# Performance work log

Hardware: AMD Instinct MI355X
Metric: run time of the kernel (lower is better)

## Reference

```python
import jax, jax.numpy as jnp
import numpy as np

D_MODEL = 1024
NUM_HEADS = 16
D_K = D_MODEL // NUM_HEADS


def setup_inputs() -> dict:
    key = jax.random.key(0)
    ks = jax.random.split(key, 5)
    s = 1.0 / np.sqrt(D_MODEL)
    return {
        "x": jax.random.normal(ks[0], (2, 2048, D_MODEL), dtype=jnp.float32),
        "Wq": jax.random.normal(ks[1], (D_MODEL, D_MODEL), dtype=jnp.float32) * s,
        "bq": jnp.zeros((D_MODEL,), dtype=jnp.float32),
        "Wk": jax.random.normal(ks[2], (D_MODEL, D_MODEL), dtype=jnp.float32) * s,
        "bk": jnp.zeros((D_MODEL,), dtype=jnp.float32),
        "Wv": jax.random.normal(ks[3], (D_MODEL, D_MODEL), dtype=jnp.float32) * s,
        "bv": jnp.zeros((D_MODEL,), dtype=jnp.float32),
        "Wo": jax.random.normal(ks[4], (D_MODEL, D_MODEL), dtype=jnp.float32) * s,
        "bo": jnp.zeros((D_MODEL,), dtype=jnp.float32),
    }


def reference(x, Wq, bq, Wk, bk, Wv, bv, Wo, bo):
    B, S, D = x.shape
    H, dk = NUM_HEADS, D_K
    Q = x @ Wq + bq  # [B, S, D]
    K = x @ Wk + bk
    V = x @ Wv + bv
    # Faithful to the torch code: plain .view(B, H, S, dk) (NO transpose),
    # i.e. heads are carved out of the flattened (S*D) dim, not the feature dim.
    Q = Q.reshape(B, H, S, dk)
    K = K.reshape(B, H, S, dk)
    V = V.reshape(B, H, S, dk)
    scores = jnp.einsum("bhqd,bhkd->bhqk", Q, K) / jnp.sqrt(jnp.float32(dk))
    attn = jax.nn.softmax(scores, axis=-1)  # [B, H, S, S]
    ctx = jnp.einsum("bhqk,bhkd->bhqd", attn, V)  # [B, H, S, dk]
    out = ctx.reshape(B, S, D) @ Wo + bo
    return out  # dropout is identity in eval mode
```

## Files before the change

kernel.cpp:

```cpp
#include <hip/hip_runtime.h>
#include <hip/hip_bf16.h>
#include <math.h>

#define D_MODEL 1024
#define SEQ     2048
#define BATCH   2
#define NHEAD   16
#define DKH     64
#define BH      (BATCH * NHEAD)

typedef unsigned short u16;
typedef unsigned int   u32;
typedef __bf16 bf16x8 __attribute__((ext_vector_type(8)));
typedef float  f32x4  __attribute__((ext_vector_type(4)));

#define MFMA16(a, b, c) __builtin_amdgcn_mfma_f32_16x16x32_bf16((a), (b), (c), 0, 0, 0)
#define AS1 __attribute__((address_space(1)))
#define AS3 __attribute__((address_space(3)))

#define QSCALE 0.18033688f

__device__ __forceinline__ u16 f2bf(float x) {
    u32 u = __float_as_uint(x);
    u += 0x7fffu + ((u >> 16) & 1u);
    return (u16)(u >> 16);
}
__device__ __forceinline__ float bf2f(u16 b) {
    return __uint_as_float(((u32)b) << 16);
}
__device__ __forceinline__ void gl16(const u16* g, void* lds) {
    __builtin_amdgcn_global_load_lds((const AS1 u32*)g, (AS3 u32*)lds, 16, 0, 0);
}

__global__ __launch_bounds__(256) void conv_all(
    const float* __restrict__ x, u16* __restrict__ Xh, int n4,
    const float* __restrict__ W0, const float* __restrict__ W1,
    const float* __restrict__ W2, const float* __restrict__ W3,
    u16* __restrict__ H0, u16* __restrict__ L0, u16* __restrict__ H1, u16* __restrict__ L1,
    u16* __restrict__ H2, u16* __restrict__ L2, u16* __restrict__ H3, u16* __restrict__ L3)
{
    const int t = threadIdx.x;
    if ((int)blockIdx.x < 4096) {
        int i = blockIdx.x * 256 + t;
        if (i >= n4) return;
        float4 v = reinterpret_cast<const float4*>(x)[i];
        uint2 H;
        H.x = f2bf(v.x) | ((u32)f2bf(v.y) << 16);
        H.y = f2bf(v.z) | ((u32)f2bf(v.w) << 16);
        reinterpret_cast<uint2*>(Xh)[i] = H;
        return;
    }
    int id = blockIdx.x - 4096;
    int bx = id & 15, by = (id >> 4) & 15, bz = id >> 8;
    const float* W; u16 *Ht, *Lt;
    if (bz == 0)      { W = W0; Ht = H0; Lt = L0; }
    else if (bz == 1) { W = W1; Ht = H1; Lt = L1; }
    else if (bz == 2) { W = W2; Ht = H2; Lt = L2; }
    else              { W = W3; Ht = H3; Lt = L3; }

    __shared__ float T[64][65];
    const int n0 = bx * 64, k0 = by * 64;
    #pragma unroll
    for (int i = 0; i < 4; ++i) {
        int f = t + i * 256;
        int kr = f >> 4, ns = (f & 15) * 4;
        float4 v = *reinterpret_cast<const float4*>(&W[(size_t)(k0 + kr) * D_MODEL + n0 + ns]);
        T[kr][ns + 0] = v.x; T[kr][ns + 1] = v.y; T[kr][ns + 2] = v.z; T[kr][ns + 3] = v.w;
    }
    __syncthreads();
    #pragma unroll
    for (int i = 0; i < 4; ++i) {
        int f = t + i * 256;
        int nr = f >> 4, ks = (f & 15) * 4;
        u16 hh[4], ll[4];
        #pragma unroll
        for (int j = 0; j < 4; ++j) {
            float xv = T[ks + j][nr];
            u16 hb = f2bf(xv);
            hh[j] = hb;
            ll[j] = f2bf(xv - bf2f(hb));
        }
        uint2 H, L;
        H.x = hh[0] | ((u32)hh[1] << 16); H.y = hh[2] | ((u32)hh[3] << 16);
        L.x = ll[0] | ((u32)ll[1] << 16); L.y = ll[2] | ((u32)ll[3] << 16);
        size_t o = (size_t)(n0 + nr) * D_MODEL + k0 + ks;
        *reinterpret_cast<uint2*>(&Ht[o]) = H;
        *reinterpret_cast<uint2*>(&Lt[o]) = L;
    }
}

__global__ __launch_bounds__(512, 2) void gemm_qkv(
    const u16* __restrict__ AhG,
    const u16* __restrict__ Bqh, const u16* __restrict__ Bql,
    const u16* __restrict__ Bkh, const u16* __restrict__ Bkl,
    const u16* __restrict__ Bvh, const u16* __restrict__ Bvl,
    const float* __restrict__ bq, const float* __restrict__ bk, const float* __restrict__ bv,
    u16* __restrict__ Qb, u16* __restrict__ Kb, u16* __restrict__ Vb)
{
    constexpr int K = D_MODEL, N = D_MODEL;
    __shared__ u16 LB[2][28672];

    const int tid  = threadIdx.x;
    const int wv   = tid >> 6;
    const int lane = tid & 63;
    const int quad = lane >> 4;
    const int l16  = lane & 15;
    const int wm   = wv >> 1, wn = wv & 1;
    const int brow = blockIdx.y * 128, bcol = blockIdx.x * 128;

    const u16* sp[7];
    int sldb[7];
    #pragma unroll
    for (int j = 0; j < 7; ++j) {
        int c = wv * 7 + j, a = c >> 3, cc = c & 7;
        int row = cc * 16 + (lane >> 2);
        int gseg = (lane & 3) ^ ((lane >> 3) & 3);
        const u16* p;
        if (a == 0)      p = AhG;
        else if (a == 1) p = Bqh;
        else if (a == 2) p = Bql;
        else if (a == 3) p = Bkh;
        else if (a == 4) p = Bkl;
        else if (a == 5) p = Bvh;
        else             p = Bvl;
        int rbase = (a == 0) ? brow : bcol;
        sp[j]   = p + (size_t)(rbase + row) * K + gseg * 8;
        sldb[j] = a * 8192 + cc * 1024;
    }

    int aro[2], bro[4];
    #pragma unroll
    for (int i = 0; i < 2; ++i) {
        int mr = wm * 32 + i * 16 + l16;
        aro[i] = mr * 64 + ((quad ^ ((mr >> 1) & 3)) * 16);
    }
    #pragma unroll
    for (int i = 0; i < 4; ++i) {
        int nr = wn * 64 + i * 16 + l16;
        bro[i] = nr * 64 + ((quad ^ ((nr >> 1) & 3)) * 16);
    }

    f32x4 acc[3][2][4] = {};

    #pragma unroll
    for (int j = 0; j < 7; ++j)
        gl16(sp[j], (char*)LB[0] + sldb[j]);

    for (int it = 0; it < K / 32; ++it) {
        const int cur = it & 1;
        __syncthreads();
        if (it + 1 < K / 32) {
            const int nxt = cur ^ 1;
            const int k1 = (it + 1) * 32;
            #pragma unroll
            for (int j = 0; j < 7; ++j)
                gl16(sp[j] + k1, (char*)LB[nxt] + sldb[j]);
        }

        bf16x8 ah[2];
        #pragma unroll
        for (int i = 0; i < 2; ++i)
            ah[i] = *reinterpret_cast<const bf16x8*>((const char*)LB[cur] + aro[i]);
        #pragma unroll
        for (int m = 0; m < 3; ++m) {
            const int bbh = (1 + 2 * m) * 8192, bbl = (2 + 2 * m) * 8192;
            bf16x8 bh[4], bl[4];
            #pragma unroll
            for (int i = 0; i < 4; ++i) {
                bh[i] = *reinterpret_cast<const bf16x8*>((const char*)LB[cur] + bbh + bro[i]);
                bl[i] = *reinterpret_cast<const bf16x8*>((const char*)LB[cur] + bbl + bro[i]);
            }
            #pragma unroll
            for (int mi = 0; mi < 2; ++mi)
                #pragma unroll
                for (int ni = 0; ni < 4; ++ni) {
                    f32x4 c = acc[m][mi][ni];
                    c = MFMA16(ah[mi], bh[ni], c);
                    c = MFMA16(ah[mi], bl[ni], c);
                    acc[m][mi][ni] = c;
                }
        }
    }

    #pragma unroll
    for (int m = 0; m < 3; ++m) {
        const float* bias = (m == 0) ? bq : (m == 1) ? bk : bv;
        u16* out = (m == 0) ? Qb : (m == 1) ? Kb : Vb;
        const float sc = (m == 0) ? QSCALE : 1.0f;
        #pragma unroll
        for (int mi = 0; mi < 2; ++mi) {
            #pragma unroll
            for (int ni = 0; ni < 4; ++ni) {
                int col = bcol + wn * 64 + ni * 16 + l16;
                float bvv = bias[col];
                #pragma unroll
                for (int r = 0; r < 4; ++r) {
                    int row = brow + wm * 32 + mi * 16 + quad * 4 + r;
                    out[(size_t)row * N + col] = f2bf((acc[m][mi][ni][r] + bvv) * sc);
                }
            }
        }
    }
}

__global__ __launch_bounds__(512, 2) void gemm_oproj(
    const u16* __restrict__ AhG, const u16* __restrict__ Bh, const u16* __restrict__ Bl,
    const float* __restrict__ bias, float* __restrict__ Cf)
{
    constexpr int K = D_MODEL, N = D_MODEL;
    __shared__ u16 LB[2][12288];

    const int tid  = threadIdx.x;
    const int wv   = tid >> 6;
    const int lane = tid & 63;
    const int quad = lane >> 4;
    const int l16  = lane & 15;
    const int wm   = wv >> 1, wn = wv & 1;
    const int brow = blockIdx.y * 128, bcol = blockIdx.x * 128;

    const u16* sp[3];
    int sldb[3];
    #pragma unroll
    for (int j = 0; j < 3; ++j) {
        int c = wv * 3 + j, a = c >> 3, cc = c & 7;
        int row = cc * 16 + (lane >> 2);
        int gseg = (lane & 3) ^ ((lane >> 3) & 3);
        const u16* p = (a == 0) ? AhG : (a == 1) ? Bh : Bl;
        int rbase = (a == 0) ? brow : bcol;
        sp[j]   = p + (size_t)(rbase + row) * K + gseg * 8;
        sldb[j] = a * 8192 + cc * 1024;
    }

    int aro[2], bro[4];
    #pragma unroll
    for (int i = 0; i < 2; ++i) {
        int mr = wm * 32 + i * 16 + l16;
        aro[i] = mr * 64 + ((quad ^ ((mr >> 1) & 3)) * 16);
    }
    #pragma unroll
    for (int i = 0; i < 4; ++i) {
        int nr = wn * 64 + i * 16 + l16;
        bro[i] = nr * 64 + ((quad ^ ((nr >> 1) & 3)) * 16);
    }

    f32x4 acc[2][4] = {};

    #pragma unroll
    for (int j = 0; j < 3; ++j)
        gl16(sp[j], (char*)LB[0] + sldb[j]);

    for (int it = 0; it < K / 32; ++it) {
        const int cur = it & 1;
        __syncthreads();
        if (it + 1 < K / 32) {
            const int nxt = cur ^ 1;
            const int k1 = (it + 1) * 32;
            #pragma unroll
            for (int j = 0; j < 3; ++j)
                gl16(sp[j] + k1, (char*)LB[nxt] + sldb[j]);
        }

        bf16x8 ah[2], bh[4], bl[4];
        #pragma unroll
        for (int i = 0; i < 2; ++i)
            ah[i] = *reinterpret_cast<const bf16x8*>((const char*)LB[cur] + aro[i]);
        #pragma unroll
        for (int i = 0; i < 4; ++i) {
            bh[i] = *reinterpret_cast<const bf16x8*>((const char*)LB[cur] + 8192 + bro[i]);
            bl[i] = *reinterpret_cast<const bf16x8*>((const char*)LB[cur] + 16384 + bro[i]);
        }
        #pragma unroll
        for (int mi = 0; mi < 2; ++mi)
            #pragma unroll
            for (int ni = 0; ni < 4; ++ni) {
                f32x4 c = acc[mi][ni];
                c = MFMA16(ah[mi], bh[ni], c);
                c = MFMA16(ah[mi], bl[ni], c);
                acc[mi][ni] = c;
            }
    }

    #pragma unroll
    for (int mi = 0; mi < 2; ++mi) {
        #pragma unroll
        for (int ni = 0; ni < 4; ++ni) {
            int col = bcol + wn * 64 + ni * 16 + l16;
            float bvv = bias[col];
            #pragma unroll
            for (int r = 0; r < 4; ++r) {
                int row = brow + wm * 32 + mi * 16 + quad * 4 + r;
                Cf[(size_t)row * N + col] = acc[mi][ni][r] + bvv;
            }
        }
    }
}

__global__ __launch_bounds__(256) void v_transpose(
    const u16* __restrict__ V, u16* __restrict__ Vt)
{
    __shared__ u16 T[64][72];
    const int bh = blockIdx.y, st = blockIdx.x;
    const u16* src = V + ((size_t)bh * SEQ + (size_t)st * 64) * 64;
    const int t = threadIdx.x;
    #pragma unroll
    for (int i = 0; i < 2; ++i) {
        int c  = t + i * 256;
        int s  = c >> 3;
        int d0 = (c & 7) * 8;
        uint4 v = reinterpret_cast<const uint4*>(src)[c];
        u16 e[8];
        e[0] = (u16)(v.x & 0xffff); e[1] = (u16)(v.x >> 16);
        e[2] = (u16)(v.y & 0xffff); e[3] = (u16)(v.y >> 16);
        e[4] = (u16)(v.z & 0xffff); e[5] = (u16)(v.z >> 16);
        e[6] = (u16)(v.w & 0xffff); e[7] = (u16)(v.w >> 16);
        #pragma unroll
        for (int j = 0; j < 8; ++j) T[d0 + j][s] = e[j];
    }
    __syncthreads();
    const int d = t >> 2, seg = t & 3;
    u16* dst = Vt + (size_t)bh * 64 * SEQ + (size_t)d * SEQ + st * 64 + seg * 16;
    uint4 a = *reinterpret_cast<const uint4*>(&T[d][seg * 16]);
    uint4 b = *reinterpret_cast<const uint4*>(&T[d][seg * 16 + 8]);
    reinterpret_cast<uint4*>(dst)[0] = a;
    reinterpret_cast<uint4*>(dst)[1] = b;
}

__global__ __launch_bounds__(256, 2) void attn_mfma(
    const u16* __restrict__ Qb_g, const u16* __restrict__ Kb_g,
    const u16* __restrict__ Vt_g, u16* __restrict__ Ch_g)
{
    __shared__ u16 KVS[2][8192];
    __shared__ u16 Pb [128 * 72];

    const int tid  = threadIdx.x;
    const int wv   = tid >> 6;
    const int lane = tid & 63;
    const int quad = lane >> 4;
    const int l16  = lane & 15;
    const int id   = blockIdx.x;
    const int bh   = id & 31;
    const int qt   = id >> 5;

    const size_t qbase = ((size_t)bh * SEQ + (size_t)qt * 128) * 64;
    const size_t kbh   = (size_t)bh * SEQ * 64;
    const size_t vtbh  = (size_t)bh * 64 * SEQ;

    bf16x8 qf[2][2];
    #pragma unroll
    for (int sub = 0; sub < 2; ++sub)
        #pragma unroll
        for (int ks = 0; ks < 2; ++ks) {
            size_t o = qbase + (size_t)(wv * 32 + sub * 16 + l16) * 64 + ks * 32 + quad * 8;
            qf[sub][ks] = *reinterpret_cast<const bf16x8*>(Qb_g + o);
        }

    const u16* sp[4];
    size_t sstep[4];
    int sldb[4];
    #pragma unroll
    for (int j = 0; j < 4; ++j) {
        int c   = wv * 4 + j;
        int arr = c >> 3, cc = c & 7;
        int row = cc * 8 + (lane >> 3);
        int sg  = (lane & 7) ^ (row & 7);
        if (arr == 0) { sp[j] = Kb_g + kbh + (size_t)row * 64 + sg * 8;   sstep[j] = 4096; }
        else          { sp[j] = Vt_g + vtbh + (size_t)row * SEQ + sg * 8; sstep[j] = 64; }
        sldb[j] = arr * 8192 + cc * 1024;
    }

    int fro[4][2];
    #pragma unroll
    for (int t = 0; t < 4; ++t)
        #pragma unroll
        for (int ks = 0; ks < 2; ++ks)
            fro[t][ks] = (t * 16 + l16) * 128 + (((ks * 4 + quad) ^ (l16 & 7)) * 16);

    bf16x8 onesv;
    #pragma unroll
    for (int i = 0; i < 8; ++i) onesv[i] = (__bf16)1.0f;

    f32x4 oacc[2][4] = {};
    f32x4 lsum[2] = {};

    #pragma unroll
    for (int j = 0; j < 4; ++j)
        gl16(sp[j], (char*)KVS[0] + sldb[j]);

    for (int kt = 0; kt < SEQ / 64; ++kt) {
        const int cur = kt & 1;
        __syncthreads();
        if (kt + 1 < SEQ / 64) {
            const int nxt = cur ^ 1;
            #pragma unroll
            for (int j = 0; j < 4; ++j)
                gl16(sp[j] + (size_t)(kt + 1) * sstep[j], (char*)KVS[nxt] + sldb[j]);
        }

        f32x4 sacc[2][4] = {};
        #pragma unroll
        for (int t4 = 0; t4 < 4; ++t4) {
            bf16x8 kh[2];
            kh[0] = *reinterpret_cast<const bf16x8*>((const char*)KVS[cur] + fro[t4][0]);
            kh[1] = *reinterpret_cast<const bf16x8*>((const char*)KVS[cur] + fro[t4][1]);
            #pragma unroll
            for (int sub = 0; sub < 2; ++sub) {
                f32x4 a = sacc[sub][t4];
                a = MFMA16(qf[sub][0], kh[0], a);
                a = MFMA16(qf[sub][1], kh[1], a);
                sacc[sub][t4] = a;
            }
        }

        #pragma unroll
        for (int sub = 0; sub < 2; ++sub) {
            int rowb = wv * 32 + sub * 16 + quad * 4;
            #pragma unroll
            for (int r = 0; r < 4; ++r) {
                u32 u0 = __float_as_uint(__builtin_amdgcn_exp2f(sacc[sub][0][r]));
                u32 u1 = __float_as_uint(__builtin_amdgcn_exp2f(sacc[sub][1][r]));
                u32 u2 = __float_as_uint(__builtin_amdgcn_exp2f(sacc[sub][2][r]));
                u32 u3 = __float_as_uint(__builtin_amdgcn_exp2f(sacc[sub][3][r]));
                int ro = (rowb + r) * 72 + l16;
                Pb[ro +  0] = (u16)(u0 >> 16);
                Pb[ro + 16] = (u16)(u1 >> 16);
                Pb[ro + 32] = (u16)(u2 >> 16);
                Pb[ro + 48] = (u16)(u3 >> 16);
            }
        }

        bf16x8 bvf[4][2];
        #pragma unroll
        for (int dt = 0; dt < 4; ++dt) {
            bvf[dt][0] = *reinterpret_cast<const bf16x8*>((const char*)KVS[cur] + 8192 + fro[dt][0]);
            bvf[dt][1] = *reinterpret_cast<const bf16x8*>((const char*)KVS[cur] + 8192 + fro[dt][1]);
        }
        #pragma unroll
        for (int sub = 0; sub < 2; ++sub) {
            bf16x8 ap[2];
            #pragma unroll
            for (int ks = 0; ks < 2; ++ks)
                ap[ks] = *reinterpret_cast<const bf16x8*>(
                    &Pb[(wv * 32 + sub * 16 + l16) * 72 + ks * 32 + quad * 8]);
            #pragma unroll
            for (int dt = 0; dt < 4; ++dt) {
                oacc[sub][dt] = MFMA16(ap[0], bvf[dt][0], oacc[sub][dt]);
                oacc[sub][dt] = MFMA16(ap[1], bvf[dt][1], oacc[sub][dt]);
            }
            lsum[sub] = MFMA16(ap[0], onesv, lsum[sub]);
            lsum[sub] = MFMA16(ap[1], onesv, lsum[sub]);
        }
    }

    u16* Oh = Ch_g + qbase;
    #pragma unroll
    for (int sub = 0; sub < 2; ++sub) {
        float inv[4];
        #pragma unroll
        for (int r = 0; r < 4; ++r) inv[r] = 1.0f / lsum[sub][r];
        #pragma unroll
        for (int dt = 0; dt < 4; ++dt)
            #pragma unroll
            for (int r = 0; r < 4; ++r) {
                int row = wv * 32 + sub * 16 + quad * 4 + r;
                Oh[(size_t)row * 64 + dt * 16 + l16] = f2bf(oacc[sub][dt][r] * inv[r]);
            }
    }
}

extern "C" void kernel_launch(void* const* d_in, const int* in_sizes, int n_in,
                              void* d_out, int out_size, void* d_ws, size_t ws_size,
                              hipStream_t stream)
{
    const float* x  = (const float*)d_in[0];
    const float* Wq = (const float*)d_in[1];
    const float* bq = (const float*)d_in[2];
    const float* Wk = (const float*)d_in[3];
    const float* bk = (const float*)d_in[4];
    const float* Wv = (const float*)d_in[5];
    const float* bv = (const float*)d_in[6];
    const float* Wo = (const float*)d_in[7];
    const float* bo = (const float*)d_in[8];
    float* out = (float*)d_out;

    const int M = BATCH * SEQ;
    const int N = D_MODEL;
    const size_t NE = (size_t)M * N;
    const size_t NW = (size_t)N * N;

    u16* w16 = (u16*)d_ws;
    u16* Xh   = w16;
    u16* Qb   = Xh   + NE;
    u16* Kb   = Qb   + NE;
    u16* Vb   = Kb   + NE;
    u16* Vtb  = Vb   + NE;
    u16* Ctxh = Vtb  + NE;
    u16* WTqh = Ctxh + NE;
    u16* WTql = WTqh + NW;
    u16* WTkh = WTql + NW;
    u16* WTkl = WTkh + NW;
    u16* WTvh = WTkl + NW;
    u16* WTvl = WTvh + NW;
    u16* WToh = WTvl + NW;
    u16* WTol = WToh + NW;

    conv_all<<<dim3(4096 + 1024), dim3(256), 0, stream>>>(
        x, Xh, (int)(NE / 4),
        Wq, Wk, Wv, Wo, WTqh, WTql, WTkh, WTkl, WTvh, WTvl, WToh, WTol);

    gemm_qkv<<<dim3(N / 128, M / 128), dim3(512), 0, stream>>>(
        Xh, WTqh, WTql, WTkh, WTkl, WTvh, WTvl, bq, bk, bv, Qb, Kb, Vb);

    v_transpose<<<dim3(SEQ / 64, BH), dim3(256), 0, stream>>>(Vb, Vtb);

    attn_mfma<<<dim3((SEQ / 128) * BH), dim3(256), 0, stream>>>(Qb, Kb, Vtb, Ctxh);

    gemm_oproj<<<dim3(N / 128, M / 128), dim3(512), 0, stream>>>(
        Ctxh, WToh, WTol, bo, out);
}
```

Baseline: 224.5 us.

## Software-pipeline attention loop: overlap QK^T of next tile with PV of previous

Restructures the attention main loop so each iteration computes the scores of the current K tile and the P·V product of the previous tile back to back, then does the exp2 and P write. The K/V staging buffer grows from double to triple buffering so prefetch, current and previous tiles coexist. It also raises wave priority around the MFMA phases with s_setprio. The aim is to hide exp and LDS latency behind matrix work, at the cost of more LDS per block, which could limit occupancy.

```diff
diff --git a/kernel.cpp b/kernel.cpp
--- a/kernel.cpp
+++ b/kernel.cpp
@@ -329,7 +329,7 @@
     const u16* __restrict__ Qb_g, const u16* __restrict__ Kb_g,
     const u16* __restrict__ Vt_g, u16* __restrict__ Ch_g)
 {
-    __shared__ u16 KVS[2][8192];
+    __shared__ u16 KVS[3][8192];
     __shared__ u16 Pb [128 * 72];
 
     const int tid  = threadIdx.x;
@@ -382,35 +382,48 @@
     f32x4 oacc[2][4] = {};
     f32x4 lsum[2] = {};
 
-    #pragma unroll
-    for (int j = 0; j < 4; ++j)
-        gl16(sp[j], (char*)KVS[0] + sldb[j]);
-
-    for (int kt = 0; kt < SEQ / 64; ++kt) {
-        const int cur = kt & 1;
-        __syncthreads();
-        if (kt + 1 < SEQ / 64) {
-            const int nxt = cur ^ 1;
-            #pragma unroll
-            for (int j = 0; j < 4; ++j)
-                gl16(sp[j] + (size_t)(kt + 1) * sstep[j], (char*)KVS[nxt] + sldb[j]);
-        }
-
-        f32x4 sacc[2][4] = {};
+    auto S_step = [&](int bufidx, f32x4 (&sacc)[2][4]) {
+        const char* kb = (const char*)KVS[bufidx];
         #pragma unroll
         for (int t4 = 0; t4 < 4; ++t4) {
-            bf16x8 kh[2];
-            kh[0] = *reinterpret_cast<const bf16x8*>((const char*)KVS[cur] + fro[t4][0]);
-            kh[1] = *reinterpret_cast<const bf16x8*>((const char*)KVS[cur] + fro[t4][1]);
+            bf16x8 kh0 = *reinterpret_cast<const bf16x8*>(kb + fro[t4][0]);
+            bf16x8 kh1 = *reinterpret_cast<const bf16x8*>(kb + fro[t4][1]);
             #pragma unroll
             for (int sub = 0; sub < 2; ++sub) {
                 f32x4 a = sacc[sub][t4];
-                a = MFMA16(qf[sub][0], kh[0], a);
-                a = MFMA16(qf[sub][1], kh[1], a);
+                a = MFMA16(qf[sub][0], kh0, a);
+                a = MFMA16(qf[sub][1], kh1, a);
                 sacc[sub][t4] = a;
             }
         }
-
+    };
+
+    auto PV_step = [&](int bufidx) {
+        const char* vb = (const char*)KVS[bufidx] + 8192;
+        bf16x8 bvf[4][2];
+        #pragma unroll
+        for (int dt = 0; dt < 4; ++dt) {
+            bvf[dt][0] = *reinterpret_cast<const bf16x8*>(vb + fro[dt][0]);
+            bvf[dt][1] = *reinterpret_cast<const bf16x8*>(vb + fro[dt][1]);
+        }
+        #pragma unroll
+        for (int sub = 0; sub < 2; ++sub) {
+            bf16x8 ap[2];
+            #pragma unroll
+            for (int ks = 0; ks < 2; ++ks)
+                ap[ks] = *reinterpret_cast<const bf16x8*>(
+                    &Pb[(wv * 32 + sub * 16 + l16) * 72 + ks * 32 + quad * 8]);
+            #pragma unroll
+            for (int dt = 0; dt < 4; ++dt) {
+                oacc[sub][dt] = MFMA16(ap[0], bvf[dt][0], oacc[sub][dt]);
+                oacc[sub][dt] = MFMA16(ap[1], bvf[dt][1], oacc[sub][dt]);
+            }
+            lsum[sub] = MFMA16(ap[0], onesv, lsum[sub]);
+            lsum[sub] = MFMA16(ap[1], onesv, lsum[sub]);
+        }
+    };
+
+    auto EXP2_step = [&](f32x4 (&sacc)[2][4]) {
         #pragma unroll
         for (int sub = 0; sub < 2; ++sub) {
             int rowb = wv * 32 + sub * 16 + quad * 4;
@@ -427,29 +440,46 @@
                 Pb[ro + 48] = (u16)(u3 >> 16);
             }
         }
-
-        bf16x8 bvf[4][2];
-        #pragma unroll
-        for (int dt = 0; dt < 4; ++dt) {
-            bvf[dt][0] = *reinterpret_cast<const bf16x8*>((const char*)KVS[cur] + 8192 + fro[dt][0]);
-            bvf[dt][1] = *reinterpret_cast<const bf16x8*>((const char*)KVS[cur] + 8192 + fro[dt][1]);
-        }
-        #pragma unroll
-        for (int sub = 0; sub < 2; ++sub) {
-            bf16x8 ap[2];
-            #pragma unroll
-            for (int ks = 0; ks < 2; ++ks)
-                ap[ks] = *reinterpret_cast<const bf16x8*>(
-                    &Pb[(wv * 32 + sub * 16 + l16) * 72 + ks * 32 + quad * 8]);
-            #pragma unroll
-            for (int dt = 0; dt < 4; ++dt) {
-                oacc[sub][dt] = MFMA16(ap[0], bvf[dt][0], oacc[sub][dt]);
-                oacc[sub][dt] = MFMA16(ap[1], bvf[dt][1], oacc[sub][dt]);
-            }
-            lsum[sub] = MFMA16(ap[0], onesv, lsum[sub]);
-            lsum[sub] = MFMA16(ap[1], onesv, lsum[sub]);
-        }
-    }
+    };
+
+    #pragma unroll
+    for (int j = 0; j < 4; ++j)
+        gl16(sp[j], (char*)KVS[0] + sldb[j]);
+
+    {
+        __syncthreads();
+        #pragma unroll
+        for (int j = 0; j < 4; ++j)
+            gl16(sp[j] + sstep[j], (char*)KVS[1] + sldb[j]);
+        f32x4 sacc[2][4] = {};
+        __builtin_amdgcn_s_setprio(1);
+        S_step(0, sacc);
+        __builtin_amdgcn_s_setprio(0);
+        EXP2_step(sacc);
+    }
+
+    int cur = 1, prv = 0, nxt = 2;
+    for (int kt = 1; kt < SEQ / 64; ++kt) {
+        __syncthreads();
+        if (kt + 1 < SEQ / 64) {
+            #pragma unroll
+            for (int j = 0; j < 4; ++j)
+                gl16(sp[j] + (size_t)(kt + 1) * sstep[j], (char*)KVS[nxt] + sldb[j]);
+        }
+
+        f32x4 sacc[2][4] = {};
+        __builtin_amdgcn_s_setprio(1);
+        S_step(cur, sacc);
+        PV_step(prv);
+        __builtin_amdgcn_s_setprio(0);
+        EXP2_step(sacc);
+
+        prv = cur; cur = nxt; nxt = (nxt == 2) ? 0 : nxt + 1;
+    }
+
+    __builtin_amdgcn_s_setprio(1);
+    PV_step(prv);
+    __builtin_amdgcn_s_setprio(0);
 
     u16* Oh = Ch_g + qbase;
     #pragma unroll
```

Result: faster. 216.7 us (-3.5%).
